# Kernel tuning notes

Hardware: AMD Instinct MI355X
Metric: run time of the kernel (lower is better)

## Reference

```python
import jax, jax.numpy as jnp
import numpy as np

HIDDEN = 1024
NUM_EXPERTS = 8
TOP_K = 2


def setup_inputs() -> dict:
    key = jax.random.key(0)
    k_x, k_r, k_w1, k_w2 = jax.random.split(key, 4)
    x = jax.random.normal(k_x, (4, 2048, HIDDEN), dtype=jnp.float32)
    # router: nn.Linear(hidden, num_experts, bias=False) -> weight [E, H]
    router_w = jax.random.normal(k_r, (NUM_EXPERTS, HIDDEN), dtype=jnp.float32) * (HIDDEN ** -0.5)
    # expert FFN: Linear(H, 2H) then Linear(2H, H), stored as [E, H, 2H] and [E, 2H, H]
    w1 = jax.random.normal(k_w1, (NUM_EXPERTS, HIDDEN, 2 * HIDDEN), dtype=jnp.float32) * (HIDDEN ** -0.5)
    w2 = jax.random.normal(k_w2, (NUM_EXPERTS, 2 * HIDDEN, HIDDEN), dtype=jnp.float32) * ((2 * HIDDEN) ** -0.5)
    return {"x": x, "router_w": router_w, "w1": w1, "w2": w2}


def reference(x, router_w, w1, w2):
    bsz, seq, hidden = x.shape
    tokens = x.reshape(-1, hidden)                      # [T, H]
    logits = tokens @ router_w.T                        # [T, E]
    topk_vals, topk_idx = jax.lax.top_k(logits, TOP_K)  # [T, K]
    weights = jax.nn.softmax(topk_vals, axis=-1)        # [T, K]
    # Dense all-experts FFN (exact GELU, matching torch nn.GELU default)
    h = jnp.einsum('td,edf->etf', tokens, w1)           # [E, T, 2H]
    h = jax.nn.gelu(h, approximate=False)
    out_all = jnp.einsum('etf,efd->etd', h, w2)         # [E, T, H]
    # Gather top-k expert outputs per token and weighted-combine
    out_ted = jnp.transpose(out_all, (1, 0, 2))         # [T, E, H]
    gathered = jnp.take_along_axis(out_ted, topk_idx[:, :, None], axis=1)  # [T, K, H]
    output = jnp.sum(weights[:, :, None] * gathered, axis=1)               # [T, H]
    return output.reshape(bsz, seq, hidden)
```

## Files before the change

### kernel.cpp

```cpp
#include <hip/hip_runtime.h>
#include <cstdint>
#include <cstddef>

#define T_TOKENS 8192
#define HID 1024
#define HID2 2048
#define NE 8

typedef unsigned short u16;
typedef unsigned int u32;
typedef __bf16 bf16x8 __attribute__((ext_vector_type(8)));
typedef float f32x4 __attribute__((ext_vector_type(4)));

__device__ __forceinline__ float bf2f(u16 u) {
    union { u32 i; float f; } x; x.i = ((u32)u) << 16; return x.f;
}
__device__ __forceinline__ u16 f2bf(float f) {
    union { float f; u32 i; } x; x.f = f;
    u32 r = x.i + 0x7fffu + ((x.i >> 16) & 1u);
    return (u16)(r >> 16);
}

__device__ __forceinline__ void cp16(const void* g, void* l) {
    __builtin_amdgcn_global_load_lds(
        (const __attribute__((address_space(1))) u32*)g,
        (__attribute__((address_space(3))) u32*)l,
        16, 0, 0);
}

__device__ __forceinline__ float gelu_f(float v) {
    float v2 = v * v;
    float t = fmaf(0.0713548162726f, v2, 1.59576912161f);
    float d = 1.0f + __expf(-v * t);
    return v * __builtin_amdgcn_rcpf(d);
}

#define BAR()   asm volatile("s_barrier" ::: "memory")
#define LGKM0() asm volatile("s_waitcnt lgkmcnt(0)" ::: "memory")
#define VMC(n)  asm volatile("s_waitcnt vmcnt(" #n ")" ::: "memory")

__device__ __forceinline__ int sfun(int r) { return (r & 2) | ((r >> 2) & 1); }

__global__ __launch_bounds__(256) void router_kernel(
    const float* __restrict__ x, const float* __restrict__ rw,
    u16* __restrict__ xb,
    int* __restrict__ cnt, int* __restrict__ rowlist,
    int* __restrict__ tok_slots, float* __restrict__ tok_w)
{
    __shared__ int lbin[NE];
    __shared__ int gbase[NE];
    int tid = threadIdx.x;
    if (tid < NE) lbin[tid] = 0;
    __syncthreads();

    int wave = tid >> 6;
    int lane = tid & 63;
    int tg = lane >> 3, il = lane & 7;
    int t = blockIdx.x * 32 + wave * 8 + tg;

    const float* xrow = x + (size_t)t * HID;
    u16* xbrow = xb + (size_t)t * HID;

    float acc[NE];
#pragma unroll
    for (int e = 0; e < NE; e++) acc[e] = 0.f;

#pragma unroll 8
    for (int q = 0; q < 32; q++) {
        int c = il * 4 + 32 * q;
        float4 xv = *(const float4*)(xrow + c);
        u16 p[4] = { f2bf(xv.x), f2bf(xv.y), f2bf(xv.z), f2bf(xv.w) };
        *(uint2*)(xbrow + c) = *(const uint2*)p;
#pragma unroll
        for (int e = 0; e < NE; e++) {
            float4 rv = *(const float4*)(rw + (size_t)e * HID + c);
            acc[e] = fmaf(xv.x, rv.x, acc[e]);
            acc[e] = fmaf(xv.y, rv.y, acc[e]);
            acc[e] = fmaf(xv.z, rv.z, acc[e]);
            acc[e] = fmaf(xv.w, rv.w, acc[e]);
        }
    }
#pragma unroll
    for (int e = 0; e < NE; e++) {
        acc[e] += __shfl_xor(acc[e], 1, 64);
        acc[e] += __shfl_xor(acc[e], 2, 64);
        acc[e] += __shfl_xor(acc[e], 4, 64);
    }

    int i0 = 0, i1 = 0, ph0 = 0, ph1 = 0;
    float w0 = 0.f, w1 = 0.f;
    if (il == 0) {
        float v0 = -1e30f;
#pragma unroll
        for (int e = 0; e < NE; e++) if (acc[e] > v0) { v0 = acc[e]; i0 = e; }
        float v1 = -1e30f;
#pragma unroll
        for (int e = 0; e < NE; e++) if (e != i0 && acc[e] > v1) { v1 = acc[e]; i1 = e; }
        w0 = 1.0f / (1.0f + __expf(v1 - v0));
        w1 = 1.0f - w0;
        ph0 = atomicAdd(&lbin[i0], 1);
        ph1 = atomicAdd(&lbin[i1], 1);
    }
    __syncthreads();
    if (tid < NE) gbase[tid] = atomicAdd(&cnt[tid * 32], lbin[tid]);
    __syncthreads();
    if (il == 0) {
        int p0 = gbase[i0] + ph0;
        int p1 = gbase[i1] + ph1;
        rowlist[i0 * T_TOKENS + p0] = t;
        rowlist[i1 * T_TOKENS + p1] = t;
        tok_slots[t * 2 + 0] = (i0 << 16) | p0;
        tok_slots[t * 2 + 1] = (i1 << 16) | p1;
        tok_w[t * 2 + 0] = w0;
        tok_w[t * 2 + 1] = w1;
    }
}

#define BM 256
#define BN 256
#define BK 64
#define HLF 8192

__global__ void offsets_kernel(const int* __restrict__ cnt,
                               int* __restrict__ off, int* __restrict__ cntc,
                               int* __restrict__ tmap, int* __restrict__ ntile)
{
    if (threadIdx.x == 0) {
        int s = 0, ti = 0;
        for (int e = 0; e < NE; e++) {
            int c = cnt[e * 32];
            off[e] = s; cntc[e] = c; s += c;
            int nmt = (c + BM - 1) / BM;
            for (int m = 0; m < nmt; m++) tmap[ti++] = (e << 16) | m;
        }
        ntile[0] = ti;
    }
}

__global__ __launch_bounds__(256) void convtrans_kernel(
    const float* __restrict__ in, u16* __restrict__ outp, int K, int N)
{
    __shared__ u16 tile[64][72];
    int e = blockIdx.z;
    const float* ip = in + (size_t)e * K * N;
    u16* op = outp + (size_t)e * K * N;
    int n0 = blockIdx.x * 64, k0 = blockIdx.y * 64;
    int t = threadIdx.x;

    int k = t >> 2;
    int nq = (t & 3) * 16;
    const float* src = ip + (size_t)(k0 + k) * N + n0 + nq;
#pragma unroll
    for (int q = 0; q < 4; q++) {
        float4 v = *(const float4*)(src + q * 4);
        tile[nq + q * 4 + 0][k] = f2bf(v.x);
        tile[nq + q * 4 + 1][k] = f2bf(v.y);
        tile[nq + q * 4 + 2][k] = f2bf(v.z);
        tile[nq + q * 4 + 3][k] = f2bf(v.w);
    }
    __syncthreads();

    int n = t >> 2;
    int kq = (t & 3) * 16;
    u16* dst = op + (size_t)(n0 + n) * K + k0 + kq;
    *(uint4*)(dst + 0) = *(const uint4*)&tile[n][kq + 0];
    *(uint4*)(dst + 8) = *(const uint4*)&tile[n][kq + 8];
}

__global__ __launch_bounds__(512, 2) void gemm1_kernel(
    const u16* __restrict__ xb, const u16* __restrict__ w1t,
    const int* __restrict__ cntc, const int* __restrict__ off,
    const int* __restrict__ rowlist, const int* __restrict__ tmap,
    const int* __restrict__ ntile, u16* __restrict__ hbuf)
{
    __shared__ u16 AsF[4 * HLF];
    __shared__ u16 BsF[4 * HLF];
    __shared__ int toks[BM];

    int id = blockIdx.x;
    int swz = (id & 7) * 72 + (id >> 3);
    int bt = swz >> 3, nt = swz & 7;
    if (bt >= ntile[0]) return;
    int em = tmap[bt];
    int e = em >> 16, mt = em & 0xffff;
    int n_e = cntc[e];

    int tid = threadIdx.x;
    if (tid < BM) {
        int r = mt * BM + tid;
        if (r >= n_e) r = n_e - 1;
        toks[tid] = rowlist[e * T_TOKENS + r];
    }
    __syncthreads();

    int wv = tid >> 6, lane = tid & 63;
    int wm = (wv >> 2) * 128, wn = (wv & 3) * 64;
    int l15 = lane & 15, l4 = lane >> 4;

    int r0 = (wv * 2 + 0) * 16 + (lane >> 2);
    int r1 = (wv * 2 + 1) * 16 + (lane >> 2);
    int sl = lane & 3;
    int as0 = (sl ^ sfun(r0)) << 3;
    int as1 = (sl ^ sfun(r1)) << 3;
    int d0 = (wv * 2 + 0) * 512 + lane * 8;
    int d1 = (wv * 2 + 1) * 512 + lane * 8;
    const u16* aRow0 = xb + (size_t)toks[r0] * HID;
    const u16* aRow1 = xb + (size_t)toks[r1] * HID;
    const u16* w1e = w1t + ((size_t)e * HID2 + (size_t)nt * BN) * HID;
    const u16* bRow0 = w1e + (size_t)r0 * HID;
    const u16* bRow1 = w1e + (size_t)r1 * HID;

    int aoff[8], boff[4];
#pragma unroll
    for (int i = 0; i < 8; i++) { int ra = wm + i * 16 + l15; aoff[i] = ra * 32 + ((l4 ^ sfun(ra)) << 3); }
#pragma unroll
    for (int j = 0; j < 4; j++) { int rb = wn + j * 16 + l15; boff[j] = rb * 32 + ((l4 ^ sfun(rb)) << 3); }

    f32x4 acc[8][4];
#pragma unroll
    for (int i = 0; i < 8; i++)
#pragma unroll
        for (int j = 0; j < 4; j++) acc[i][j] = (f32x4){0.f, 0.f, 0.f, 0.f};

#define ST_A(db, h, kt) do { \
    cp16(aRow0 + (kt) * BK + (h) * 32 + as0, &AsF[((db) * 2 + (h)) * HLF + d0]); \
    cp16(aRow1 + (kt) * BK + (h) * 32 + as1, &AsF[((db) * 2 + (h)) * HLF + d1]); } while (0)
#define ST_B(db, h, kt) do { \
    cp16(bRow0 + (kt) * BK + (h) * 32 + as0, &BsF[((db) * 2 + (h)) * HLF + d0]); \
    cp16(bRow1 + (kt) * BK + (h) * 32 + as1, &BsF[((db) * 2 + (h)) * HLF + d1]); } while (0)

    const int NKT = HID / BK;
    ST_A(0, 0, 0); ST_B(0, 0, 0);
    ST_A(0, 1, 0); ST_B(0, 1, 0);
    ST_A(1, 0, 1); ST_B(1, 0, 1);
    VMC(4);
    BAR();

    for (int kt = 0; kt < NKT; kt++) {
        int buf = kt & 1, nbuf = buf ^ 1;
        int base0 = (buf * 2 + 0) * HLF;
        int base1 = (buf * 2 + 1) * HLF;
        bf16x8 af[8], bq0, bq1;
#pragma unroll
        for (int i = 0; i < 8; i++) af[i] = *(const bf16x8*)&AsF[base0 + aoff[i]];
        bq0 = *(const bf16x8*)&BsF[base0 + boff[0]];
        bq1 = *(const bf16x8*)&BsF[base0 + boff[1]];
        if (kt + 1 < NKT) ST_A(nbuf, 1, kt + 1);
        BAR(); LGKM0();
        __builtin_amdgcn_s_setprio(1);
#pragma unroll
        for (int i = 0; i < 8; i++) {
            acc[i][0] = __builtin_amdgcn_mfma_f32_16x16x32_bf16(bq0, af[i], acc[i][0], 0, 0, 0);
            acc[i][1] = __builtin_amdgcn_mfma_f32_16x16x32_bf16(bq1, af[i], acc[i][1], 0, 0, 0);
        }
        __builtin_amdgcn_s_setprio(0);
        BAR();
        bq0 = *(const bf16x8*)&BsF[base0 + boff[2]];
        bq1 = *(const bf16x8*)&BsF[base0 + boff[3]];
        if (kt + 1 < NKT) ST_B(nbuf, 1, kt + 1);
        BAR(); LGKM0();
        __builtin_amdgcn_s_setprio(1);
#pragma unroll
        for (int i = 0; i < 8; i++) {
            acc[i][2] = __builtin_amdgcn_mfma_f32_16x16x32_bf16(bq0, af[i], acc[i][2], 0, 0, 0);
            acc[i][3] = __builtin_amdgcn_mfma_f32_16x16x32_bf16(bq1, af[i], acc[i][3], 0, 0, 0);
        }
        __builtin_amdgcn_s_setprio(0);
        BAR();
#pragma unroll
        for (int i = 0; i < 8; i++) af[i] = *(const bf16x8*)&AsF[base1 + aoff[i]];
        bq0 = *(const bf16x8*)&BsF[base1 + boff[0]];
        bq1 = *(const bf16x8*)&BsF[base1 + boff[1]];
        if (kt + 2 < NKT) ST_A(buf, 0, kt + 2);
        BAR(); LGKM0();
        __builtin_amdgcn_s_setprio(1);
#pragma unroll
        for (int i = 0; i < 8; i++) {
            acc[i][0] = __builtin_amdgcn_mfma_f32_16x16x32_bf16(bq0, af[i], acc[i][0], 0, 0, 0);
            acc[i][1] = __builtin_amdgcn_mfma_f32_16x16x32_bf16(bq1, af[i], acc[i][1], 0, 0, 0);
        }
        __builtin_amdgcn_s_setprio(0);
        BAR();
        bq0 = *(const bf16x8*)&BsF[base1 + boff[2]];
        bq1 = *(const bf16x8*)&BsF[base1 + boff[3]];
        if (kt + 2 < NKT) ST_B(buf, 0, kt + 2);
        BAR(); LGKM0();
        __builtin_amdgcn_s_setprio(1);
#pragma unroll
        for (int i = 0; i < 8; i++) {
            acc[i][2] = __builtin_amdgcn_mfma_f32_16x16x32_bf16(bq0, af[i], acc[i][2], 0, 0, 0);
            acc[i][3] = __builtin_amdgcn_mfma_f32_16x16x32_bf16(bq1, af[i], acc[i][3], 0, 0, 0);
        }
        __builtin_amdgcn_s_setprio(0);
        if (kt + 2 < NKT)      { VMC(4); }
        else if (kt + 1 < NKT) { VMC(0); }
        BAR();
    }
#undef ST_A
#undef ST_B

    int base_row = off[e] + mt * BM;
#pragma unroll
    for (int i = 0; i < 8; i++) {
        int m = wm + i * 16 + l15;
        int r = mt * BM + m;
        if (r < n_e) {
            u16* orow = hbuf + (size_t)(base_row + m) * HID2 + nt * BN + wn + l4 * 4;
#pragma unroll
            for (int j = 0; j < 4; j++) {
                u16 p[4];
#pragma unroll
                for (int rg = 0; rg < 4; rg++) p[rg] = f2bf(gelu_f(acc[i][j][rg]));
                *(uint2*)(orow + j * 16) = *(const uint2*)p;
            }
        }
    }
}

__global__ __launch_bounds__(512, 2) void gemm2_kernel(
    const u16* __restrict__ hbuf, const u16* __restrict__ w2t,
    const int* __restrict__ cntc, const int* __restrict__ off,
    const int* __restrict__ tmap, const int* __restrict__ ntile,
    u16* __restrict__ ybuf)
{
    __shared__ u16 AsF[4 * HLF];
    __shared__ u16 BsF[4 * HLF];

    int id = blockIdx.x;
    int swz = (id & 7) * 36 + (id >> 3);
    int bt = swz >> 2, nt = swz & 3;
    if (bt >= ntile[0]) return;
    int em = tmap[bt];
    int e = em >> 16, mt = em & 0xffff;
    int n_e = cntc[e];

    int tid = threadIdx.x;
    int wv = tid >> 6, lane = tid & 63;
    int wm = (wv >> 2) * 128, wn = (wv & 3) * 64;
    int l15 = lane & 15, l4 = lane >> 4;

    int r0 = (wv * 2 + 0) * 16 + (lane >> 2);
    int r1 = (wv * 2 + 1) * 16 + (lane >> 2);
    int sl = lane & 3;
    int as0 = (sl ^ sfun(r0)) << 3;
    int as1 = (sl ^ sfun(r1)) << 3;
    int d0 = (wv * 2 + 0) * 512 + lane * 8;
    int d1 = (wv * 2 + 1) * 512 + lane * 8;
    const u16* hrow = hbuf + (size_t)(off[e] + mt * BM) * HID2;
    const u16* aRow0 = hrow + (size_t)r0 * HID2;
    const u16* aRow1 = hrow + (size_t)r1 * HID2;
    const u16* w2e = w2t + ((size_t)e * HID + (size_t)nt * BN) * HID2;
    const u16* bRow0 = w2e + (size_t)r0 * HID2;
    const u16* bRow1 = w2e + (size_t)r1 * HID2;

    int aoff[8], boff[4];
#pragma unroll
    for (int i = 0; i < 8; i++) { int ra = wm + i * 16 + l15; aoff[i] = ra * 32 + ((l4 ^ sfun(ra)) << 3); }
#pragma unroll
    for (int j = 0; j < 4; j++) { int rb = wn + j * 16 + l15; boff[j] = rb * 32 + ((l4 ^ sfun(rb)) << 3); }

    f32x4 acc[8][4];
#pragma unroll
    for (int i = 0; i < 8; i++)
#pragma unroll
        for (int j = 0; j < 4; j++) acc[i][j] = (f32x4){0.f, 0.f, 0.f, 0.f};

#define ST_A(db, h, kt) do { \
    cp16(aRow0 + (kt) * BK + (h) * 32 + as0, &AsF[((db) * 2 + (h)) * HLF + d0]); \
    cp16(aRow1 + (kt) * BK + (h) * 32 + as1, &AsF[((db) * 2 + (h)) * HLF + d1]); } while (0)
#define ST_B(db, h, kt) do { \
    cp16(bRow0 + (kt) * BK + (h) * 32 + as0, &BsF[((db) * 2 + (h)) * HLF + d0]); \
    cp16(bRow1 + (kt) * BK + (h) * 32 + as1, &BsF[((db) * 2 + (h)) * HLF + d1]); } while (0)

    const int NKT = HID2 / BK;
    ST_A(0, 0, 0); ST_B(0, 0, 0);
    ST_A(0, 1, 0); ST_B(0, 1, 0);
    ST_A(1, 0, 1); ST_B(1, 0, 1);
    VMC(4);
    BAR();

    for (int kt = 0; kt < NKT; kt++) {
        int buf = kt & 1, nbuf = buf ^ 1;
        int base0 = (buf * 2 + 0) * HLF;
        int base1 = (buf * 2 + 1) * HLF;
        bf16x8 af[8], bq0, bq1;
#pragma unroll
        for (int i = 0; i < 8; i++) af[i] = *(const bf16x8*)&AsF[base0 + aoff[i]];
        bq0 = *(const bf16x8*)&BsF[base0 + boff[0]];
        bq1 = *(const bf16x8*)&BsF[base0 + boff[1]];
        if (kt + 1 < NKT) ST_A(nbuf, 1, kt + 1);
        BAR(); LGKM0();
        __builtin_amdgcn_s_setprio(1);
#pragma unroll
        for (int i = 0; i < 8; i++) {
            acc[i][0] = __builtin_amdgcn_mfma_f32_16x16x32_bf16(bq0, af[i], acc[i][0], 0, 0, 0);
            acc[i][1] = __builtin_amdgcn_mfma_f32_16x16x32_bf16(bq1, af[i], acc[i][1], 0, 0, 0);
        }
        __builtin_amdgcn_s_setprio(0);
        BAR();
        bq0 = *(const bf16x8*)&BsF[base0 + boff[2]];
        bq1 = *(const bf16x8*)&BsF[base0 + boff[3]];
        if (kt + 1 < NKT) ST_B(nbuf, 1, kt + 1);
        BAR(); LGKM0();
        __builtin_amdgcn_s_setprio(1);
#pragma unroll
        for (int i = 0; i < 8; i++) {
            acc[i][2] = __builtin_amdgcn_mfma_f32_16x16x32_bf16(bq0, af[i], acc[i][2], 0, 0, 0);
            acc[i][3] = __builtin_amdgcn_mfma_f32_16x16x32_bf16(bq1, af[i], acc[i][3], 0, 0, 0);
        }
        __builtin_amdgcn_s_setprio(0);
        BAR();
#pragma unroll
        for (int i = 0; i < 8; i++) af[i] = *(const bf16x8*)&AsF[base1 + aoff[i]];
        bq0 = *(const bf16x8*)&BsF[base1 + boff[0]];
        bq1 = *(const bf16x8*)&BsF[base1 + boff[1]];
        if (kt + 2 < NKT) ST_A(buf, 0, kt + 2);
        BAR(); LGKM0();
        __builtin_amdgcn_s_setprio(1);
#pragma unroll
        for (int i = 0; i < 8; i++) {
            acc[i][0] = __builtin_amdgcn_mfma_f32_16x16x32_bf16(bq0, af[i], acc[i][0], 0, 0, 0);
            acc[i][1] = __builtin_amdgcn_mfma_f32_16x16x32_bf16(bq1, af[i], acc[i][1], 0, 0, 0);
        }
        __builtin_amdgcn_s_setprio(0);
        BAR();
        bq0 = *(const bf16x8*)&BsF[base1 + boff[2]];
        bq1 = *(const bf16x8*)&BsF[base1 + boff[3]];
        if (kt + 2 < NKT) ST_B(buf, 0, kt + 2);
        BAR(); LGKM0();
        __builtin_amdgcn_s_setprio(1);
#pragma unroll
        for (int i = 0; i < 8; i++) {
            acc[i][2] = __builtin_amdgcn_mfma_f32_16x16x32_bf16(bq0, af[i], acc[i][2], 0, 0, 0);
            acc[i][3] = __builtin_amdgcn_mfma_f32_16x16x32_bf16(bq1, af[i], acc[i][3], 0, 0, 0);
        }
        __builtin_amdgcn_s_setprio(0);
        if (kt + 2 < NKT)      { VMC(4); }
        else if (kt + 1 < NKT) { VMC(0); }
        BAR();
    }
#undef ST_A
#undef ST_B

    int base_row = off[e] + mt * BM;
#pragma unroll
    for (int i = 0; i < 8; i++) {
        int m = wm + i * 16 + l15;
        int r = mt * BM + m;
        if (r < n_e) {
            u16* orow = ybuf + (size_t)(base_row + m) * HID + nt * BN + wn + l4 * 4;
#pragma unroll
            for (int j = 0; j < 4; j++) {
                u16 p[4];
#pragma unroll
                for (int rg = 0; rg < 4; rg++) p[rg] = f2bf(acc[i][j][rg]);
                *(uint2*)(orow + j * 16) = *(const uint2*)p;
            }
        }
    }
}

__global__ __launch_bounds__(256) void combine_kernel(
    const u16* __restrict__ ybuf, const int* __restrict__ off,
    const int* __restrict__ tok_slots, const float* __restrict__ tok_w,
    float* __restrict__ out)
{
    int tid = threadIdx.x;
    int t = blockIdx.x * 2 + (tid >> 7);
    int c = (tid & 127) * 8;
    int s0 = tok_slots[t * 2], s1 = tok_slots[t * 2 + 1];
    float w0 = tok_w[t * 2], w1 = tok_w[t * 2 + 1];
    int r0 = off[s0 >> 16] + (s0 & 0xFFFF);
    int r1 = off[s1 >> 16] + (s1 & 0xFFFF);
    uint4 a = *(const uint4*)(ybuf + (size_t)r0 * HID + c);
    uint4 b = *(const uint4*)(ybuf + (size_t)r1 * HID + c);
    const u16* pa = (const u16*)&a;
    const u16* pb = (const u16*)&b;
    float o[8];
#pragma unroll
    for (int q = 0; q < 8; q++) o[q] = w0 * bf2f(pa[q]) + w1 * bf2f(pb[q]);
    *(float4*)(out + (size_t)t * HID + c) = *(const float4*)&o[0];
    *(float4*)(out + (size_t)t * HID + c + 4) = *(const float4*)&o[4];
}

extern "C" void kernel_launch(void* const* d_in, const int* in_sizes, int n_in,
                              void* d_out, int out_size, void* d_ws, size_t ws_size,
                              hipStream_t stream)
{
    const float* x  = (const float*)d_in[0];
    const float* rw = (const float*)d_in[1];
    const float* w1 = (const float*)d_in[2];
    const float* w2 = (const float*)d_in[3];
    float* out = (float*)d_out;

    char* ws = (char*)d_ws;
    int*   cnt       = (int*)(ws + 0);
    int*   off       = (int*)(ws + 1024);
    int*   cntc      = (int*)(ws + 1088);
    int*   tmap      = (int*)(ws + 1152);
    int*   ntile     = (int*)(ws + 1536);
    int*   rowlist   = (int*)(ws + 2048);
    int*   tok_slots = (int*)(ws + 2048 + 262144);
    float* tok_w     = (float*)(ws + 2048 + 262144 + 65536);
    u16*   xb        = (u16*)(ws + (1ull << 20));
    u16*   wt        = (u16*)(ws + (17ull << 20));
    u16*   hbuf      = (u16*)(ws + (49ull << 20));
    u16*   ybuf      = (u16*)(ws + (114ull << 20));

    hipMemsetAsync(cnt, 0, 1024, stream);

    router_kernel<<<T_TOKENS / 32, 256, 0, stream>>>(x, rw, xb, cnt, rowlist, tok_slots, tok_w);
    offsets_kernel<<<1, 64, 0, stream>>>(cnt, off, cntc, tmap, ntile);

    convtrans_kernel<<<dim3(HID2 / 64, HID / 64, NE), 256, 0, stream>>>(w1, wt, HID, HID2);
    gemm1_kernel<<<72 * (HID2 / BN), 512, 0, stream>>>(xb, wt, cntc, off, rowlist, tmap, ntile, hbuf);

    convtrans_kernel<<<dim3(HID / 64, HID2 / 64, NE), 256, 0, stream>>>(w2, wt, HID2, HID);
    gemm2_kernel<<<72 * (HID / BN), 512, 0, stream>>>(hbuf, wt, cntc, off, tmap, ntile, ybuf);

    combine_kernel<<<T_TOKENS / 2, 256, 0, stream>>>(ybuf, off, tok_slots, tok_w, out);
}
```

Measured before the change: 477.3 us.

## Software-pipeline LDS fragment loads with MFMA and halve barriers in MoE GEMMs

After: 490.0 us. 1.03x slower.

```diff
diff --git a/kernel.cpp b/kernel.cpp
--- a/kernel.cpp
+++ b/kernel.cpp
@@ -35,9 +35,10 @@
     return v * __builtin_amdgcn_rcpf(d);
 }
 
-#define BAR()   asm volatile("s_barrier" ::: "memory")
-#define LGKM0() asm volatile("s_waitcnt lgkmcnt(0)" ::: "memory")
-#define VMC(n)  asm volatile("s_waitcnt vmcnt(" #n ")" ::: "memory")
+#define BAR()    asm volatile("s_barrier" ::: "memory")
+#define VMC(n)   asm volatile("s_waitcnt vmcnt(" #n ")" ::: "memory")
+#define LGKMC(n) asm volatile("s_waitcnt lgkmcnt(" #n ")" ::: "memory")
+#define SDB()    __builtin_amdgcn_sched_barrier(0)
 
 __device__ __forceinline__ int sfun(int r) { return (r & 2) | ((r >> 2) & 1); }
 
@@ -167,6 +168,15 @@
     *(uint4*)(dst + 8) = *(const uint4*)&tile[n][kq + 8];
 }
 
+#define PR_A4(dst, bb, lo) do { _Pragma("unroll") \
+    for (int _i = 0; _i < 4; _i++) dst[_i] = *(const bf16x8*)&AsF[(bb) + aoff[(lo) + _i]]; } while (0)
+#define PR_B4(dst, bb) do { _Pragma("unroll") \
+    for (int _j = 0; _j < 4; _j++) dst[_j] = *(const bf16x8*)&BsF[(bb) + boff[_j]]; } while (0)
+#define MF16(AF, BQ, R0) do { _Pragma("unroll") \
+    for (int _i = 0; _i < 4; _i++) { _Pragma("unroll") \
+      for (int _j = 0; _j < 4; _j++) \
+        acc[(R0) + _i][_j] = __builtin_amdgcn_mfma_f32_16x16x32_bf16(BQ[_j], AF[_i], acc[(R0) + _i][_j], 0, 0, 0); } } while (0)
+
 __global__ __launch_bounds__(512, 2) void gemm1_kernel(
     const u16* __restrict__ xb, const u16* __restrict__ w1t,
     const int* __restrict__ cntc, const int* __restrict__ off,
@@ -233,67 +243,40 @@
     ST_A(0, 0, 0); ST_B(0, 0, 0);
     ST_A(0, 1, 0); ST_B(0, 1, 0);
     ST_A(1, 0, 1); ST_B(1, 0, 1);
-    VMC(4);
+    VMC(6);
     BAR();
+    bf16x8 afA[4], afB[4], bqA[4], bqB[4];
+    PR_A4(afA, 0, 0); PR_B4(bqA, 0);
 
     for (int kt = 0; kt < NKT; kt++) {
         int buf = kt & 1, nbuf = buf ^ 1;
-        int base0 = (buf * 2 + 0) * HLF;
-        int base1 = (buf * 2 + 1) * HLF;
-        bf16x8 af[8], bq0, bq1;
-#pragma unroll
-        for (int i = 0; i < 8; i++) af[i] = *(const bf16x8*)&AsF[base0 + aoff[i]];
-        bq0 = *(const bf16x8*)&BsF[base0 + boff[0]];
-        bq1 = *(const bf16x8*)&BsF[base0 + boff[1]];
+        int b0 = (buf * 2 + 0) * HLF;
+        int b1 = (buf * 2 + 1) * HLF;
+        int nb0 = (nbuf * 2 + 0) * HLF;
+        VMC(4);
+        PR_A4(afB, b0, 4);
         if (kt + 1 < NKT) ST_A(nbuf, 1, kt + 1);
-        BAR(); LGKM0();
-        __builtin_amdgcn_s_setprio(1);
-#pragma unroll
-        for (int i = 0; i < 8; i++) {
-            acc[i][0] = __builtin_amdgcn_mfma_f32_16x16x32_bf16(bq0, af[i], acc[i][0], 0, 0, 0);
-            acc[i][1] = __builtin_amdgcn_mfma_f32_16x16x32_bf16(bq1, af[i], acc[i][1], 0, 0, 0);
-        }
-        __builtin_amdgcn_s_setprio(0);
-        BAR();
-        bq0 = *(const bf16x8*)&BsF[base0 + boff[2]];
-        bq1 = *(const bf16x8*)&BsF[base0 + boff[3]];
+        LGKMC(4); SDB();
+        __builtin_amdgcn_s_setprio(1); MF16(afA, bqA, 0); __builtin_amdgcn_s_setprio(0);
+        BAR();
+        VMC(4);
+        PR_A4(afA, b1, 0); PR_B4(bqB, b1);
         if (kt + 1 < NKT) ST_B(nbuf, 1, kt + 1);
-        BAR(); LGKM0();
-        __builtin_amdgcn_s_setprio(1);
-#pragma unroll
-        for (int i = 0; i < 8; i++) {
-            acc[i][2] = __builtin_amdgcn_mfma_f32_16x16x32_bf16(bq0, af[i], acc[i][2], 0, 0, 0);
-            acc[i][3] = __builtin_amdgcn_mfma_f32_16x16x32_bf16(bq1, af[i], acc[i][3], 0, 0, 0);
-        }
-        __builtin_amdgcn_s_setprio(0);
-        BAR();
-#pragma unroll
-        for (int i = 0; i < 8; i++) af[i] = *(const bf16x8*)&AsF[base1 + aoff[i]];
-        bq0 = *(const bf16x8*)&BsF[base1 + boff[0]];
-        bq1 = *(const bf16x8*)&BsF[base1 + boff[1]];
+        LGKMC(8); SDB();
+        __builtin_amdgcn_s_setprio(1); MF16(afB, bqA, 4); __builtin_amdgcn_s_setprio(0);
+        BAR();
+        VMC(4);
+        PR_A4(afB, b1, 4);
         if (kt + 2 < NKT) ST_A(buf, 0, kt + 2);
-        BAR(); LGKM0();
-        __builtin_amdgcn_s_setprio(1);
-#pragma unroll
-        for (int i = 0; i < 8; i++) {
-            acc[i][0] = __builtin_amdgcn_mfma_f32_16x16x32_bf16(bq0, af[i], acc[i][0], 0, 0, 0);
-            acc[i][1] = __builtin_amdgcn_mfma_f32_16x16x32_bf16(bq1, af[i], acc[i][1], 0, 0, 0);
-        }
-        __builtin_amdgcn_s_setprio(0);
-        BAR();
-        bq0 = *(const bf16x8*)&BsF[base1 + boff[2]];
-        bq1 = *(const bf16x8*)&BsF[base1 + boff[3]];
+        LGKMC(4); SDB();
+        __builtin_amdgcn_s_setprio(1); MF16(afA, bqB, 0); __builtin_amdgcn_s_setprio(0);
+        BAR();
+        VMC(4);
+        if (kt + 1 < NKT) { PR_A4(afA, nb0, 0); PR_B4(bqA, nb0); }
         if (kt + 2 < NKT) ST_B(buf, 0, kt + 2);
-        BAR(); LGKM0();
-        __builtin_amdgcn_s_setprio(1);
-#pragma unroll
-        for (int i = 0; i < 8; i++) {
-            acc[i][2] = __builtin_amdgcn_mfma_f32_16x16x32_bf16(bq0, af[i], acc[i][2], 0, 0, 0);
-            acc[i][3] = __builtin_amdgcn_mfma_f32_16x16x32_bf16(bq1, af[i], acc[i][3], 0, 0, 0);
-        }
-        __builtin_amdgcn_s_setprio(0);
-        if (kt + 2 < NKT)      { VMC(4); }
-        else if (kt + 1 < NKT) { VMC(0); }
+        if (kt + 1 < NKT) { LGKMC(8); } else { LGKMC(0); }
+        SDB();
+        __builtin_amdgcn_s_setprio(1); MF16(afB, bqB, 4); __builtin_amdgcn_s_setprio(0);
         BAR();
     }
 #undef ST_A
@@ -376,67 +359,40 @@
     ST_A(0, 0, 0); ST_B(0, 0, 0);
     ST_A(0, 1, 0); ST_B(0, 1, 0);
     ST_A(1, 0, 1); ST_B(1, 0, 1);
-    VMC(4);
+    VMC(6);
     BAR();
+    bf16x8 afA[4], afB[4], bqA[4], bqB[4];
+    PR_A4(afA, 0, 0); PR_B4(bqA, 0);
 
     for (int kt = 0; kt < NKT; kt++) {
         int buf = kt & 1, nbuf = buf ^ 1;
-        int base0 = (buf * 2 + 0) * HLF;
-        int base1 = (buf * 2 + 1) * HLF;
-        bf16x8 af[8], bq0, bq1;
-#pragma unroll
-        for (int i = 0; i < 8; i++) af[i] = *(const bf16x8*)&AsF[base0 + aoff[i]];
-        bq0 = *(const bf16x8*)&BsF[base0 + boff[0]];
-        bq1 = *(const bf16x8*)&BsF[base0 + boff[1]];
+        int b0 = (buf * 2 + 0) * HLF;
+        int b1 = (buf * 2 + 1) * HLF;
+        int nb0 = (nbuf * 2 + 0) * HLF;
+        VMC(4);
+        PR_A4(afB, b0, 4);
         if (kt + 1 < NKT) ST_A(nbuf, 1, kt + 1);
-        BAR(); LGKM0();
-        __builtin_amdgcn_s_setprio(1);
-#pragma unroll
-        for (int i = 0; i < 8; i++) {
-            acc[i][0] = __builtin_amdgcn_mfma_f32_16x16x32_bf16(bq0, af[i], acc[i][0], 0, 0, 0);
-            acc[i][1] = __builtin_amdgcn_mfma_f32_16x16x32_bf16(bq1, af[i], acc[i][1], 0, 0, 0);
-        }
-        __builtin_amdgcn_s_setprio(0);
-        BAR();
-        bq0 = *(const bf16x8*)&BsF[base0 + boff[2]];
-        bq1 = *(const bf16x8*)&BsF[base0 + boff[3]];
+        LGKMC(4); SDB();
+        __builtin_amdgcn_s_setprio(1); MF16(afA, bqA, 0); __builtin_amdgcn_s_setprio(0);
+        BAR();
+        VMC(4);
+        PR_A4(afA, b1, 0); PR_B4(bqB, b1);
         if (kt + 1 < NKT) ST_B(nbuf, 1, kt + 1);
-        BAR(); LGKM0();
-        __builtin_amdgcn_s_setprio(1);
-#pragma unroll
-        for (int i = 0; i < 8; i++) {
-            acc[i][2] = __builtin_amdgcn_mfma_f32_16x16x32_bf16(bq0, af[i], acc[i][2], 0, 0, 0);
-            acc[i][3] = __builtin_amdgcn_mfma_f32_16x16x32_bf16(bq1, af[i], acc[i][3], 0, 0, 0);
-        }
-        __builtin_amdgcn_s_setprio(0);
-        BAR();
-#pragma unroll
-        for (int i = 0; i < 8; i++) af[i] = *(const bf16x8*)&AsF[base1 + aoff[i]];
-        bq0 = *(const bf16x8*)&BsF[base1 + boff[0]];
-        bq1 = *(const bf16x8*)&BsF[base1 + boff[1]];
+        LGKMC(8); SDB();
+        __builtin_amdgcn_s_setprio(1); MF16(afB, bqA, 4); __builtin_amdgcn_s_setprio(0);
+        BAR();
+        VMC(4);
+        PR_A4(afB, b1, 4);
         if (kt + 2 < NKT) ST_A(buf, 0, kt + 2);
-        BAR(); LGKM0();
-        __builtin_amdgcn_s_setprio(1);
-#pragma unroll
-        for (int i = 0; i < 8; i++) {
-            acc[i][0] = __builtin_amdgcn_mfma_f32_16x16x32_bf16(bq0, af[i], acc[i][0], 0, 0, 0);
-            acc[i][1] = __builtin_amdgcn_mfma_f32_16x16x32_bf16(bq1, af[i], acc[i][1], 0, 0, 0);
-        }
-        __builtin_amdgcn_s_setprio(0);
-        BAR();
-        bq0 = *(const bf16x8*)&BsF[base1 + boff[2]];
-        bq1 = *(const bf16x8*)&BsF[base1 + boff[3]];
+        LGKMC(4); SDB();
+        __builtin_amdgcn_s_setprio(1); MF16(afA, bqB, 0); __builtin_amdgcn_s_setprio(0);
+        BAR();
+        VMC(4);
+        if (kt + 1 < NKT) { PR_A4(afA, nb0, 0); PR_B4(bqA, nb0); }
         if (kt + 2 < NKT) ST_B(buf, 0, kt + 2);
-        BAR(); LGKM0();
-        __builtin_amdgcn_s_setprio(1);
-#pragma unroll
-        for (int i = 0; i < 8; i++) {
-            acc[i][2] = __builtin_amdgcn_mfma_f32_16x16x32_bf16(bq0, af[i], acc[i][2], 0, 0, 0);
-            acc[i][3] = __builtin_amdgcn_mfma_f32_16x16x32_bf16(bq1, af[i], acc[i][3], 0, 0, 0);
-        }
-        __builtin_amdgcn_s_setprio(0);
-        if (kt + 2 < NKT)      { VMC(4); }
-        else if (kt + 1 < NKT) { VMC(0); }
+        if (kt + 1 < NKT) { LGKMC(8); } else { LGKMC(0); }
+        SDB();
+        __builtin_amdgcn_s_setprio(1); MF16(afB, bqB, 4); __builtin_amdgcn_s_setprio(0);
         BAR();
     }
 #undef ST_A
```
